# Kernel tuning notes

Hardware: AMD Instinct MI355X
Metric: run time of the kernel (lower is better)

## Reference

```python
import jax, jax.numpy as jnp
import numpy as np

B = 4; IMG = 32; P = 2; CIN = 3; G = IMG // P; N = G * G; D = 768; NL = 8
DI = 1536; NH = 24; HD = 64; DS = 128; CONVDIM = DI + 2 * DS; DPROJ = 2 * DI + 2 * DS + NH
OUTC = 3 * CIN; FREQ = 256; EPS = 1e-6


def _sincos_1d(dim, pos):
    omega = np.arange(dim // 2, dtype=np.float64) / (dim / 2.0)
    omega = 1.0 / 10000 ** omega
    out = np.einsum('m,d->md', pos.reshape(-1), omega)
    return np.concatenate([np.sin(out), np.cos(out)], axis=1)


def _pos_embed_2d(dim, gs):
    gh = np.arange(gs, dtype=np.float32)
    gw = np.arange(gs, dtype=np.float32)
    grid = np.stack(np.meshgrid(gw, gh), axis=0)
    return np.concatenate([_sincos_1d(dim // 2, grid[0]), _sincos_1d(dim // 2, grid[1])], axis=1)


POS = jnp.asarray(_pos_embed_2d(D, G), dtype=jnp.float32)[None]  # [1, N, D]


def _ln(x):
    m = x.mean(-1, keepdims=True)
    v = ((x - m) ** 2).mean(-1, keepdims=True)
    return (x - m) * jax.lax.rsqrt(v + EPS)


def _patch_embed(img, w, b):
    # conv with kernel=stride=P == reshape to (c, ph, pw)-ordered patch vectors + matmul
    xp = img.reshape(B, CIN, G, P, G, P).transpose(0, 2, 4, 1, 3, 5).reshape(B, N, CIN * P * P)
    return xp @ w + b


def _t_embed(t, tw1, tb1, tw2, tb2):
    half = FREQ // 2
    freqs = jnp.exp(-jnp.log(10000.0) * jnp.arange(half, dtype=jnp.float32) / half)
    args = t[:, None] * freqs[None]
    emb = jnp.concatenate([jnp.cos(args), jnp.sin(args)], axis=-1)
    return jax.nn.silu(emb @ tw1 + tb1) @ tw2 + tb2


def _mamba2(u, in_w, conv_w, conv_b, dt_bias, A_log, D_ssm, out_w):
    # u: [B, N, D]
    zxbcdt = u @ in_w                           # [B, N, DPROJ]
    z = zxbcdt[..., :DI]
    xBC = zxbcdt[..., DI:DI + CONVDIM]
    dt_raw = zxbcdt[..., DI + CONVDIM:]
    # causal depthwise conv1d, kernel 4
    pad = jnp.pad(xBC, ((0, 0), (3, 0), (0, 0)))
    xBC = sum(pad[:, k:k + N, :] * conv_w[:, k] for k in range(4)) + conv_b
    xBC = jax.nn.silu(xBC)
    xs = xBC[..., :DI].reshape(B, N, NH, HD)
    Bm = xBC[..., DI:DI + DS]
    Cm = xBC[..., DI + DS:]
    dt = jax.nn.softplus(dt_raw + dt_bias)       # [B, N, NH]
    a = dt * (-jnp.exp(A_log))                   # [B, N, NH], negative
    acum = jnp.cumsum(a, axis=1)
    seg = acum[:, :, None, :] - acum[:, None, :, :]   # [B, l, s, NH]
    tril = jnp.tril(jnp.ones((N, N), bool))
    decay = jnp.exp(jnp.where(tril[None, :, :, None], seg, -1e30))
    decay = jnp.moveaxis(decay, -1, 1)           # [B, NH, l, s]
    CB = jnp.einsum('bln,bsn->bls', Cm, Bm)
    scores = CB[:, None] * decay * jnp.moveaxis(dt, -1, 1)[:, :, None, :]
    y = jnp.einsum('bhls,bshp->blhp', scores, xs) + D_ssm[None, None, :, None] * xs
    y = y.reshape(B, N, DI) * jax.nn.silu(z)
    return y @ out_w


def _conv3(x, w, b):
    o = jax.lax.conv_general_dilated(x, w, (1, 1), 'SAME',
                                     dimension_numbers=('NCHW', 'OIHW', 'NCHW'))
    return o + b[None, :, None, None]


def _hfnet(h, w1, b1, w2, b2, w3, b3):
    c = jax.nn.relu(_conv3(h, w1, b1))
    c = jax.nn.relu(_conv3(c, w2, b2))
    return h + _conv3(c, w3, b3)


def _forward(x, t, y, H1, H2, H3, xe_w, xe_b, ye_w, ye_b, tw1, tb1, tw2, tb2,
             adaln_w, adaln_b, in_w, conv_w, conv_b, dt_bias, A_log, D_ssm, out_w,
             fl_t_w, fl_t_b, fl_y_w, fl_y_b, fl_lin_w, fl_lin_b,
             e1_w1, e1_b1, e1_w2, e1_b2, e1_w3, e1_b3,
             e2_w1, e2_b1, e2_w2, e2_b2, e2_w3, e2_b3,
             e3_w1, e3_b1, e3_w2, e3_b2, e3_w3, e3_b3):
    xe = _patch_embed(x, xe_w, xe_b) + POS
    ye = _patch_embed(y, ye_w, ye_b) + POS
    te = _t_embed(t, tw1, tb1, tw2, tb2)
    st = jax.nn.silu(te)          # [B, D]
    sy = jax.nn.silu(ye)          # [B, N, D]

    def layer(xc, p):
        aw, ab, iw, cw, cb, db, al, dd, ow = p
        sh_t, sc_t, g_t = jnp.split(st @ aw + ab, 3, axis=-1)
        sh_y, sc_y, g_y = jnp.split(sy @ aw + ab, 3, axis=-1)
        shift = sh_t[:, None] + sh_y
        scale = sc_t[:, None] + sc_y
        gate = g_t[:, None] + g_y
        xm = _ln(xc) * (1.0 + scale) + shift
        return gate * _mamba2(xm, iw, cw, cb, db, al, dd, ow) + xc, None

    xh, _ = jax.lax.scan(layer, xe, (adaln_w, adaln_b, in_w, conv_w, conv_b,
                                     dt_bias, A_log, D_ssm, out_w))
    sh_t, sc_t = jnp.split(st @ fl_t_w + fl_t_b, 2, axis=-1)
    sh_y, sc_y = jnp.split(sy @ fl_y_w + fl_y_b, 2, axis=-1)
    xf = (_ln(xh) * (1.0 + sc_t[:, None] + sc_y) + sh_t[:, None] + sh_y) @ fl_lin_w + fl_lin_b
    # unpatchify: nhwpqc -> nchpwq
    img = xf.reshape(B, G, G, P, P, OUTC).transpose(0, 5, 1, 3, 2, 4).reshape(B, OUTC, IMG, IMG)
    h1 = _hfnet(H1, e1_w1, e1_b1, e1_w2, e1_b2, e1_w3, e1_b3)
    h2 = _hfnet(H2, e2_w1, e2_b1, e2_w2, e2_b2, e2_w3, e2_b3)
    h3 = _hfnet(H3, e3_w1, e3_b1, e3_w2, e3_b2, e3_w3, e3_b3)
    return (img, h1, h2, h3)


def setup_inputs() -> dict:
    ks = iter(jax.random.split(jax.random.key(0), 80))
    def nrm(shape, s=0.02):
        return jax.random.normal(next(ks), shape, jnp.float32) * s
    z = lambda *s: jnp.zeros(s, jnp.float32)
    inp = {}
    inp['x'] = jax.random.normal(next(ks), (B, CIN, IMG, IMG), jnp.float32)
    inp['t'] = jax.random.uniform(next(ks), (B,), jnp.float32) * 1000.0
    inp['y'] = jax.random.normal(next(ks), (B, CIN, IMG, IMG), jnp.float32)
    inp['H1'] = jax.random.normal(next(ks), (B, CIN, IMG, IMG), jnp.float32)
    inp['H2'] = jax.random.normal(next(ks), (B, CIN, IMG, IMG), jnp.float32)
    inp['H3'] = jax.random.normal(next(ks), (B, CIN, IMG, IMG), jnp.float32)
    inp['xe_w'] = nrm((CIN * P * P, D), 0.1); inp['xe_b'] = z(D)
    inp['ye_w'] = nrm((CIN * P * P, D), 0.1); inp['ye_b'] = z(D)
    inp['tw1'] = nrm((FREQ, D)); inp['tb1'] = z(D)
    inp['tw2'] = nrm((D, D)); inp['tb2'] = z(D)
    inp['adaln_w'] = nrm((NL, D, 3 * D)); inp['adaln_b'] = nrm((NL, 3 * D))
    inp['in_w'] = nrm((NL, D, DPROJ))
    inp['conv_w'] = nrm((NL, CONVDIM, 4), 0.2); inp['conv_b'] = z(NL, CONVDIM)
    inp['dt_bias'] = nrm((NL, NH), 0.5)
    inp['A_log'] = jnp.tile(jnp.log(jnp.arange(1.0, NH + 1.0, dtype=jnp.float32)), (NL, 1))
    inp['D_ssm'] = jnp.ones((NL, NH), jnp.float32)
    inp['out_w'] = nrm((NL, DI, D))
    inp['fl_t_w'] = nrm((D, 2 * D)); inp['fl_t_b'] = z(2 * D)
    inp['fl_y_w'] = nrm((D, 2 * D)); inp['fl_y_b'] = z(2 * D)
    inp['fl_lin_w'] = nrm((D, P * P * OUTC)); inp['fl_lin_b'] = z(P * P * OUTC)
    for i in (1, 2, 3):
        inp['e%d_w1' % i] = nrm((64, CIN, 3, 3), 0.1); inp['e%d_b1' % i] = z(64)
        inp['e%d_w2' % i] = nrm((64, 64, 3, 3), 0.05); inp['e%d_b2' % i] = z(64)
        inp['e%d_w3' % i] = nrm((CIN, 64, 3, 3), 0.05); inp['e%d_b3' % i] = z(CIN)
    return inp


def reference(x, t, y, H1, H2, H3, xe_w, xe_b, ye_w, ye_b, tw1, tb1, tw2, tb2,
              adaln_w, adaln_b, in_w, conv_w, conv_b, dt_bias, A_log, D_ssm, out_w,
              fl_t_w, fl_t_b, fl_y_w, fl_y_b, fl_lin_w, fl_lin_b,
              e1_w1, e1_b1, e1_w2, e1_b2, e1_w3, e1_b3,
              e2_w1, e2_b1, e2_w2, e2_b2, e2_w3, e2_b3,
              e3_w1, e3_b1, e3_w2, e3_b2, e3_w3, e3_b3):
    return _forward(x, t, y, H1, H2, H3, xe_w, xe_b, ye_w, ye_b, tw1, tb1, tw2, tb2,
                    adaln_w, adaln_b, in_w, conv_w, conv_b, dt_bias, A_log, D_ssm, out_w,
                    fl_t_w, fl_t_b, fl_y_w, fl_y_b, fl_lin_w, fl_lin_b,
                    e1_w1, e1_b1, e1_w2, e1_b2, e1_w3, e1_b3,
                    e2_w1, e2_b1, e2_w2, e2_b2, e2_w3, e2_b3,
                    e3_w1, e3_b1, e3_w2, e3_b2, e3_w3, e3_b3)
```

## Files before the change

### kernel.cpp

```cpp
#include <hip/hip_runtime.h>
#include <cmath>

namespace {

constexpr int kB = 4;
constexpr int kN = 256;
constexpr int kD = 768;
constexpr int kNL = 8;
constexpr int kDI = 1536;
constexpr int kNH = 24;
constexpr int kHD = 64;
constexpr int kCONV = 1792;
constexpr int kDPROJ = 3352;
constexpr int kD3 = 2304;
constexpr int kNCAT = 19968;
constexpr int kOFF_FL = 18432;

typedef __attribute__((ext_vector_type(8))) short short8;
typedef __attribute__((ext_vector_type(4))) float f32x4;

__device__ __forceinline__ float siluf(float x) { return x / (1.f + expf(-x)); }

__device__ __forceinline__ short f2bf(float f) {
  unsigned u = __float_as_uint(f);
  unsigned r = (u + 0x7fffu + ((u >> 16) & 1u)) >> 16;
  return (short)r;
}

__device__ __forceinline__ void gload_lds16(const void* g, void* l) {
  __builtin_amdgcn_global_load_lds(
      (const __attribute__((address_space(1))) void*)g,
      (__attribute__((address_space(3))) void*)l, 16, 0, 0);
}

template <int N> __device__ __forceinline__ void wait_barrier();
template <> __device__ __forceinline__ void wait_barrier<0>() {
  asm volatile("s_waitcnt vmcnt(0)\n\ts_barrier" ::: "memory");
}
template <> __device__ __forceinline__ void wait_barrier<2>() {
  asm volatile("s_waitcnt vmcnt(2)\n\ts_barrier" ::: "memory");
}
template <> __device__ __forceinline__ void wait_barrier<3>() {
  asm volatile("s_waitcnt vmcnt(3)\n\ts_barrier" ::: "memory");
}
template <> __device__ __forceinline__ void wait_barrier<4>() {
  asm volatile("s_waitcnt vmcnt(4)\n\ts_barrier" ::: "memory");
}

__global__ void patch_embed2_kernel(const float* __restrict__ img0,
                                    const float* __restrict__ w0,
                                    const float* __restrict__ b0,
                                    float* __restrict__ out0,
                                    const float* __restrict__ img1,
                                    const float* __restrict__ w1,
                                    const float* __restrict__ b1,
                                    float* __restrict__ out1,
                                    short* __restrict__ out1_bf) {
  int gid = blockIdx.x * blockDim.x + threadIdx.x;
  if (gid >= kB * kN * kD) return;
  int z = blockIdx.z;
  const float* img = z ? img1 : img0;
  const float* w = z ? w1 : w0;
  const float* bias = z ? b1 : b0;
  int d = gid % kD;
  int n = (gid / kD) % kN;
  int b = gid / (kD * kN);
  int gi = n >> 4, gj = n & 15;
  float acc = bias[d];
#pragma unroll
  for (int c = 0; c < 3; ++c)
#pragma unroll
    for (int pi = 0; pi < 2; ++pi)
#pragma unroll
      for (int pj = 0; pj < 2; ++pj) {
        float v = img[((b * 3 + c) * 32 + gi * 2 + pi) * 32 + gj * 2 + pj];
        acc += v * w[(c * 4 + pi * 2 + pj) * kD + d];
      }
  float pos;
  if (d < 192)       pos = sinf((float)gj * powf(10000.f, -(float)d / 192.f));
  else if (d < 384)  pos = cosf((float)gj * powf(10000.f, -(float)(d - 192) / 192.f));
  else if (d < 576)  pos = sinf((float)gi * powf(10000.f, -(float)(d - 384) / 192.f));
  else               pos = cosf((float)gi * powf(10000.f, -(float)(d - 576) / 192.f));
  acc += pos;
  if (z) {
    float v = siluf(acc);
    out1[gid] = v;
    out1_bf[gid] = f2bf(v);
  } else {
    out0[gid] = acc;
  }
}

__global__ void tembed_args_kernel(const float* __restrict__ t,
                                   float* __restrict__ ctst) {
  int idx = blockIdx.x * 256 + threadIdx.x;
  if (idx >= kB * 256) return;
  int b = idx >> 8, j = idx & 255;
  int k = j & 127;
  float f = expf(-9.210340371976184f * (float)k / 128.f);
  float arg = t[b] * f;
  ctst[idx] = (j < 128) ? cosf(arg) : sinf(arg);
}

__global__ __launch_bounds__(256) void splitk_mm_stage1(
    const float* __restrict__ A, const float* __restrict__ W,
    float* __restrict__ part, int K, int Nn, int KC) {
  int n = blockIdx.x * 256 + threadIdx.x;
  int kc = blockIdx.y;
  int l = blockIdx.z;
  if (n >= Nn) return;
  const float* w = W + (size_t)l * K * Nn + (size_t)kc * 64 * Nn + n;
  int kb = kc * 64;
  float a0 = 0.f, a1 = 0.f, a2 = 0.f, a3 = 0.f;
  for (int k = 0; k < 64; ++k) {
    float wv = w[(size_t)k * Nn];
    a0 += A[0 * K + kb + k] * wv;
    a1 += A[1 * K + kb + k] * wv;
    a2 += A[2 * K + kb + k] * wv;
    a3 += A[3 * K + kb + k] * wv;
  }
  size_t base = (((size_t)l * KC + kc) * 4) * Nn + n;
  part[base] = a0;
  part[base + Nn] = a1;
  part[base + 2 * (size_t)Nn] = a2;
  part[base + 3 * (size_t)Nn] = a3;
}

__global__ void splitk_mm_reduce(const float* __restrict__ part,
                                 const float* __restrict__ bias,
                                 float* __restrict__ C, int Nn, int KC, int L,
                                 int act) {
  int idx = blockIdx.x * 256 + threadIdx.x;
  if (idx >= L * 4 * Nn) return;
  int n = idx % Nn;
  int b = (idx / Nn) & 3;
  int l = idx / (4 * Nn);
  float s = bias[(size_t)l * Nn + n];
  for (int kc = 0; kc < KC; ++kc)
    s += part[(((size_t)l * KC + kc) * 4 + b) * Nn + n];
  C[idx] = act ? siluf(s) : s;
}

__global__ __launch_bounds__(256) void transposeW_kernel(
    const float* __restrict__ W, short* __restrict__ Wt, int K, int N,
    size_t sW, size_t sWt) {
  W += (size_t)blockIdx.z * sW;
  Wt += (size_t)blockIdx.z * sWt;
  __shared__ float tile[32][33];
  int n0 = blockIdx.x * 32, k0 = blockIdx.y * 32;
  int tid = threadIdx.x;
  int tx = tid & 31, ty = tid >> 5;
#pragma unroll
  for (int i = 0; i < 4; ++i) {
    int k = k0 + ty + i * 8;
    int n = n0 + tx;
    tile[ty + i * 8][tx] = (n < N) ? W[(size_t)k * N + n] : 0.f;
  }
  __syncthreads();
#pragma unroll
  for (int i = 0; i < 4; ++i) {
    int n = n0 + ty + i * 8;
    int k = k0 + tx;
    Wt[(size_t)n * K + k] = f2bf(tile[tx][ty + i * 8]);
  }
}

__global__ void concat_bias_kernel(const float* __restrict__ a,
                                   const float* __restrict__ b,
                                   float* __restrict__ dst) {
  int i = blockIdx.x * 256 + threadIdx.x;
  if (i < kOFF_FL) dst[i] = a[i];
  else if (i < kNCAT) dst[i] = b[i - kOFF_FL];
}

template <int BM, int BN>
__global__ __launch_bounds__(256) void mfma_gemm(
    const short* __restrict__ A, const short* __restrict__ Bt,
    const float* __restrict__ bias, float* __restrict__ C,
    int Nn, int Ksplit, int Ktot, int ldc, size_t czstride) {
  constexpr int MI = BM / 32;
  constexpr int NJ = BN / 32;
  constexpr int LPW = BM / 64 + BN / 64;
  __shared__ short Als[3 * BM * 32];
  __shared__ short Bls[3 * BN * 32];
  int gx = gridDim.x, gy = gridDim.y;
  int nblk = gx * gy;
  int hl = blockIdx.y * gx + blockIdx.x;
  int txi, tyi;
  if ((nblk & 7) == 0) {
    int chunk = nblk >> 3;
    int s_id = (hl & 7) * chunk + (hl >> 3);
    txi = s_id / gy;
    tyi = s_id % gy;
  } else {
    txi = blockIdx.x;
    tyi = blockIdx.y;
  }
  int m0 = tyi * BM, n0 = txi * BN;
  int koff = blockIdx.z * Ksplit;
  C += (size_t)blockIdx.z * czstride;
  int tid = threadIdx.x;
  int lane = tid & 63, wid = tid >> 6;
  int wr = wid >> 1, wc = wid & 1;
  f32x4 acc[MI][NJ] = {};
  int sm = tid >> 2;
  int sk = (tid & 3) * 8;
  const int nsteps = Ksplit >> 5;
  auto stage = [&](int buf, int k0) {
#pragma unroll
    for (int h = 0; h < BM / 64; ++h)
      gload_lds16(&A[(size_t)(m0 + h * 64 + sm) * Ktot + koff + k0 + sk],
                  &Als[buf * (BM * 32) + h * 2048 + wid * 512]);
#pragma unroll
    for (int h = 0; h < BN / 64; ++h)
      gload_lds16(&Bt[(size_t)(n0 + h * 64 + sm) * Ktot + koff + k0 + sk],
                  &Bls[buf * (BN * 32) + h * 2048 + wid * 512]);
  };
  stage(0, 0);
  if (nsteps > 1) stage(1, 32);
  int cur = 0;
  for (int s = 0; s < nsteps; ++s) {
    if (s + 1 < nsteps) wait_barrier<LPW>();
    else wait_barrier<0>();
    if (s + 2 < nsteps) stage(cur == 0 ? 2 : cur - 1, (s + 2) << 5);
    short8 av[MI], bv[NJ];
#pragma unroll
    for (int mi = 0; mi < MI; ++mi)
      av[mi] = *(const short8*)&Als[cur * (BM * 32) +
                                    (wr * (BM / 2) + mi * 16 + (lane & 15)) *
                                        32 +
                                    (lane >> 4) * 8];
#pragma unroll
    for (int nj = 0; nj < NJ; ++nj)
      bv[nj] = *(const short8*)&Bls[cur * (BN * 32) +
                                    (wc * (BN / 2) + nj * 16 + (lane & 15)) *
                                        32 +
                                    (lane >> 4) * 8];
#pragma unroll
    for (int mi = 0; mi < MI; ++mi)
#pragma unroll
      for (int nj = 0; nj < NJ; ++nj)
        acc[mi][nj] = __builtin_amdgcn_mfma_f32_16x16x32_bf16(
            av[mi], bv[nj], acc[mi][nj], 0, 0, 0);
    cur = (cur == 2) ? 0 : cur + 1;
  }
#pragma unroll
  for (int mi = 0; mi < MI; ++mi)
#pragma unroll
    for (int nj = 0; nj < NJ; ++nj)
#pragma unroll
      for (int r = 0; r < 4; ++r) {
        int gm = m0 + wr * (BM / 2) + mi * 16 + (lane >> 4) * 4 + r;
        int gn = n0 + wc * (BN / 2) + nj * 16 + (lane & 15);
        if (gn >= Nn) continue;
        C[(size_t)gm * ldc + gn] = acc[mi][nj][r] + (bias ? bias[gn] : 0.f);
      }
}

__global__ __launch_bounds__(256) void cb_mfma_kernel(
    const short* __restrict__ bC, const short* __restrict__ bB,
    float* __restrict__ CBp) {
  constexpr int K = 128;
  __shared__ short Als[128 * 32];
  __shared__ short Bls[128 * 32];
  int b = blockIdx.z;
  int m0 = blockIdx.y * 128, n0 = blockIdx.x * 128;
  if (n0 >= m0 + 128) return;
  const short* A = bC + (size_t)b * 256 * K;
  const short* Bt = bB + (size_t)b * 256 * K;
  int tid = threadIdx.x;
  int lane = tid & 63, wid = tid >> 6;
  int wr = wid >> 1, wc = wid & 1;
  f32x4 acc[4][4] = {};
  int sm = tid >> 2;
  int sk = (tid & 3) * 8;
  for (int k0 = 0; k0 < K; k0 += 32) {
    __syncthreads();
    gload_lds16(&A[(size_t)(m0 + sm) * K + k0 + sk], &Als[wid * 512]);
    gload_lds16(&A[(size_t)(m0 + 64 + sm) * K + k0 + sk],
                &Als[2048 + wid * 512]);
    gload_lds16(&Bt[(size_t)(n0 + sm) * K + k0 + sk], &Bls[wid * 512]);
    gload_lds16(&Bt[(size_t)(n0 + 64 + sm) * K + k0 + sk],
                &Bls[2048 + wid * 512]);
    __syncthreads();
    short8 av[4], bv[4];
#pragma unroll
    for (int mi = 0; mi < 4; ++mi)
      av[mi] = *(const short8*)&Als[(wr * 64 + mi * 16 + (lane & 15)) * 32 +
                                    (lane >> 4) * 8];
#pragma unroll
    for (int nj = 0; nj < 4; ++nj)
      bv[nj] = *(const short8*)&Bls[(wc * 64 + nj * 16 + (lane & 15)) * 32 +
                                    (lane >> 4) * 8];
#pragma unroll
    for (int mi = 0; mi < 4; ++mi)
#pragma unroll
      for (int nj = 0; nj < 4; ++nj)
        acc[mi][nj] = __builtin_amdgcn_mfma_f32_16x16x32_bf16(
            av[mi], bv[nj], acc[mi][nj], 0, 0, 0);
  }
#pragma unroll
  for (int mi = 0; mi < 4; ++mi)
#pragma unroll
    for (int nj = 0; nj < 4; ++nj)
#pragma unroll
      for (int r = 0; r < 4; ++r) {
        int gm = m0 + wr * 64 + mi * 16 + (lane >> 4) * 4 + r;
        int gn = n0 + wc * 64 + nj * 16 + (lane & 15);
        CBp[((size_t)(b * 256 + gm)) * 256 + gn] = acc[mi][nj][r];
      }
}

__global__ __launch_bounds__(256) void ln_mod_kernel(
    const float* __restrict__ x, const float* __restrict__ tA,
    const float* __restrict__ yA, short* __restrict__ out_bf, int tstride,
    int ystride, const float* __restrict__ p0, const float* __restrict__ p1,
    const float* __restrict__ gtA, const float* __restrict__ gyA,
    float* __restrict__ xcw) {
  int row = blockIdx.x;
  int b = row >> 8;
  __shared__ float xr[kD];
  __shared__ float red[256];
  int tid = threadIdx.x;
  float s = 0.f;
  for (int i = tid; i < kD; i += 256) {
    float v = x[(size_t)row * kD + i];
    if (p0) {
      float g = gtA[b * kD3 + 2 * kD + i] +
                gyA[(size_t)row * kNCAT + 2 * kD + i];
      v += g * (p0[(size_t)row * kD + i] + p1[(size_t)row * kD + i]);
      xcw[(size_t)row * kD + i] = v;
    }
    xr[i] = v;
    s += v;
  }
  red[tid] = s;
  __syncthreads();
  for (int o = 128; o > 0; o >>= 1) {
    if (tid < o) red[tid] += red[tid + o];
    __syncthreads();
  }
  float mean = red[0] / (float)kD;
  __syncthreads();
  float s2 = 0.f;
  for (int i = tid; i < kD; i += 256) {
    float d = xr[i] - mean;
    s2 += d * d;
  }
  red[tid] = s2;
  __syncthreads();
  for (int o = 128; o > 0; o >>= 1) {
    if (tid < o) red[tid] += red[tid + o];
    __syncthreads();
  }
  float rstd = rsqrtf(red[0] / (float)kD + 1e-6f);
  for (int i = tid; i < kD; i += 256) {
    float sc = tA[b * tstride + kD + i] + yA[(size_t)row * ystride + kD + i];
    float sh = tA[b * tstride + i] + yA[(size_t)row * ystride + i];
    float v = (xr[i] - mean) * rstd * (1.f + sc) + sh;
    out_bf[(size_t)row * kD + i] = f2bf(v);
  }
}

__global__ __launch_bounds__(256) void convdt_kernel(
    const float* __restrict__ zx, const float* __restrict__ cw,
    const float* __restrict__ cb, const float* __restrict__ db,
    const float* __restrict__ al, float* __restrict__ xbc,
    short* __restrict__ bB, short* __restrict__ bC, float* __restrict__ dts,
    float* __restrict__ acum) {
  constexpr int kConvBlocks = kB * kN * kCONV / 256;
  int blk = blockIdx.x;
  if (blk < kConvBlocks) {
    int idx = blk * 256 + threadIdx.x;
    int c = idx % kCONV;
    int row = idx / kCONV;
    int n = row & 255, b = row >> 8;
    float acc = cb[c];
#pragma unroll
    for (int k = 0; k < 4; ++k) {
      int ns = n + k - 3;
      if (ns >= 0)
        acc += zx[(size_t)(b * kN + ns) * kDPROJ + kDI + c] * cw[c * 4 + k];
    }
    float v = siluf(acc);
    xbc[idx] = v;
    if (c >= kDI) {
      if (c < kDI + 128)
        bB[(size_t)row * 128 + (c - kDI)] = f2bf(v);
      else
        bC[(size_t)row * 128 + (c - kDI - 128)] = f2bf(v);
    }
  } else {
    int bh = blk - kConvBlocks;
    int b = bh / kNH, h = bh % kNH;
    int n = threadIdx.x;
    __shared__ float sb[256];
    size_t row = (size_t)(b * kN + n);
    float xv = zx[row * kDPROJ + (kDI + kCONV) + h] + db[h];
    float dt = xv > 20.f ? xv : log1pf(expf(xv));
    dts[row * kNH + h] = dt;
    float a = -expf(al[h]) * dt;
    sb[n] = a;
    __syncthreads();
    for (int off = 1; off < 256; off <<= 1) {
      float v = (n >= off) ? sb[n - off] : 0.f;
      __syncthreads();
      sb[n] += v;
      __syncthreads();
    }
    acum[row * kNH + h] = sb[n];
  }
}

__global__ __launch_bounds__(256) void ssm_y_kernel(
    const float* __restrict__ CBp, const float* __restrict__ acum,
    const float* __restrict__ dts, const float* __restrict__ xbc,
    const float* __restrict__ zx, const float* __restrict__ Dssm,
    short* __restrict__ ybuf) {
  int bh = blockIdx.z;
  int b = bh / kNH, h = bh % kNH;
  int m0 = blockIdx.y * 64;
  int tid = threadIdx.x;
  int tx = tid & 15, ty = tid >> 4;
  __shared__ float As[16][65];
  __shared__ float Xs[16][64];
  float acc[4][4] = {};
  for (int k0 = 0; k0 < kN; k0 += 16) {
    if (k0 > m0 + 63) break;
#pragma unroll
    for (int i = 0; i < 4; ++i) {
      int e = tid + i * 256;
      int m = e >> 4, k = e & 15;
      int l = m0 + m, ss = k0 + k;
      float v = 0.f;
      if (ss <= l) {
        float dec = expf(acum[(size_t)(b * kN + l) * kNH + h] -
                         acum[(size_t)(b * kN + ss) * kNH + h]);
        v = CBp[(size_t)(b * kN + l) * kN + ss] * dec *
            dts[(size_t)(b * kN + ss) * kNH + h];
      }
      As[k][m] = v;
    }
#pragma unroll
    for (int i = 0; i < 4; ++i) {
      int e = tid + i * 256;
      int k = e >> 6, n = e & 63;
      Xs[k][n] = xbc[(size_t)(b * kN + k0 + k) * kCONV + h * kHD + n];
    }
    __syncthreads();
#pragma unroll
    for (int kk = 0; kk < 16; ++kk) {
      float a[4], bb[4];
#pragma unroll
      for (int i = 0; i < 4; ++i) a[i] = As[kk][ty * 4 + i];
#pragma unroll
      for (int j = 0; j < 4; ++j) bb[j] = Xs[kk][tx * 4 + j];
#pragma unroll
      for (int i = 0; i < 4; ++i)
#pragma unroll
        for (int j = 0; j < 4; ++j) acc[i][j] += a[i] * bb[j];
    }
    __syncthreads();
  }
  float dd = Dssm[h];
#pragma unroll
  for (int i = 0; i < 4; ++i) {
    int l = m0 + ty * 4 + i;
    size_t row = (size_t)(b * kN + l);
#pragma unroll
    for (int j = 0; j < 4; ++j) {
      int p = tx * 4 + j;
      int col = h * kHD + p;
      float xs_l = xbc[row * kCONV + col];
      float yv = acc[i][j] + dd * xs_l;
      float zv = zx[row * kDPROJ + col];
      ybuf[row * kDI + col] = f2bf(yv * siluf(zv));
    }
  }
}

__global__ void unpatchify_kernel(const float* __restrict__ fpp,
                                  const float* __restrict__ bias,
                                  float* __restrict__ out) {
  constexpr int kFP = kB * kN * 36;
  int gid = blockIdx.x * 256 + threadIdx.x;
  if (gid >= kFP) return;
  int j = gid % 36;
  int row = gid / 36;
  int n = row & 255, b = row >> 8;
  int o = j % 9;
  int pj = (j / 9) & 1;
  int pi = j / 18;
  int gi = n >> 4, gj = n & 15;
  float v = fpp[gid] + fpp[kFP + gid] + fpp[2 * kFP + gid] +
            fpp[3 * kFP + gid] + bias[j];
  out[((b * 9 + o) * 32 + gi * 2 + pi) * 32 + (gj * 2 + pj)] = v;
}

__global__ __launch_bounds__(256) void conv1_kernel(
    const float* __restrict__ Ha, const float* __restrict__ Hb,
    const float* __restrict__ Hc, const float* __restrict__ wa,
    const float* __restrict__ wb, const float* __restrict__ wc,
    const float* __restrict__ ba, const float* __restrict__ bb,
    const float* __restrict__ bc, short* __restrict__ dst) {
  int gid = blockIdx.x * 256 + threadIdx.x;
  if (gid >= 3 * 4096 * 64) return;
  int oc = gid & 63;
  int px = (gid >> 6) & 4095;
  int net = gid >> 18;
  const float* in = net == 0 ? Ha : (net == 1 ? Hb : Hc);
  const float* w = net == 0 ? wa : (net == 1 ? wb : wc);
  const float* bs = net == 0 ? ba : (net == 1 ? bb : bc);
  int xx = px & 31, yy = (px >> 5) & 31, b = px >> 10;
  float acc = bs[oc];
#pragma unroll
  for (int ic = 0; ic < 3; ++ic) {
    const float* ip = in + ((size_t)(b * 3 + ic) << 10);
    const float* wp = w + (oc * 3 + ic) * 9;
#pragma unroll
    for (int ky = 0; ky < 3; ++ky) {
      int ys = yy + ky - 1;
      if (ys < 0 || ys > 31) continue;
#pragma unroll
      for (int kx = 0; kx < 3; ++kx) {
        int xs = xx + kx - 1;
        if (xs < 0 || xs > 31) continue;
        acc += ip[ys * 32 + xs] * wp[ky * 3 + kx];
      }
    }
  }
  dst[gid] = f2bf(fmaxf(acc, 0.f));
}

__global__ __launch_bounds__(256) void convw_prep_kernel(
    const float* __restrict__ w2a, const float* __restrict__ w2b,
    const float* __restrict__ w2c, const float* __restrict__ w3a,
    const float* __restrict__ w3b, const float* __restrict__ w3c,
    short* __restrict__ dst2, short* __restrict__ dst3) {
  int idx = blockIdx.x * 256 + threadIdx.x;
  if (idx >= 3 * 128 * 576) return;
  int z = blockIdx.z;
  int OC = z ? 3 : 64;
  short* dst = z ? dst3 : dst2;
  int k = idx % 576;
  int row = (idx / 576) & 127;
  int net = idx / (128 * 576);
  const float* w = z ? (net == 0 ? w3a : (net == 1 ? w3b : w3c))
                     : (net == 0 ? w2a : (net == 1 ? w2b : w2c));
  int pos = k >> 6, ic = k & 63;
  float v = (row < OC) ? w[row * 576 + ic * 9 + pos] : 0.f;
  dst[idx] = f2bf(v);
}

template <int EP>
__global__ __launch_bounds__(256) void conv_gemm(
    const short* __restrict__ src, const short* __restrict__ Btall,
    const float* __restrict__ b_a, const float* __restrict__ b_b,
    const float* __restrict__ b_c, const float* __restrict__ r_a,
    const float* __restrict__ r_b, const float* __restrict__ r_c,
    short* __restrict__ dst, float* __restrict__ outp) {
  constexpr int K = 576;
  __shared__ short Als[128 * 32];
  __shared__ short Bls[128 * 32];
  int net = blockIdx.z;
  int m0 = blockIdx.y * 128;
  const float* bias = net == 0 ? b_a : (net == 1 ? b_b : b_c);
  const float* res = net == 0 ? r_a : (net == 1 ? r_b : r_c);
  const short* Bt = Btall + (size_t)net * 128 * K;
  int tid = threadIdx.x;
  int lane = tid & 63, wid = tid >> 6;
  int wr = wid >> 1, wc = wid & 1;
  f32x4 acc[4][4] = {};
  int sm = tid >> 2;
  int sk = (tid & 3) * 8;
  for (int k0 = 0; k0 < K; k0 += 32) {
    int kk = k0 + sk;
    int pos = kk >> 6, ic0 = kk & 63;
    int ky = pos / 3 - 1, kx = pos % 3 - 1;
    uint4 a_st[2], b_st[2];
#pragma unroll
    for (int i = 0; i < 2; ++i) {
      int px = m0 + i * 64 + sm;
      int b = px >> 10;
      int yy = (px >> 5) & 31, xx = px & 31;
      int ys = yy + ky, xs = xx + kx;
      if (ys >= 0 && ys < 32 && xs >= 0 && xs < 32) {
        a_st[i] = *(const uint4*)&src[((size_t)(net * 4096 + (b << 10) +
                                                (ys << 5) + xs)
                                       << 6) +
                                      ic0];
      } else {
        a_st[i] = make_uint4(0u, 0u, 0u, 0u);
      }
      b_st[i] = *(const uint4*)&Bt[(size_t)(i * 64 + sm) * K + kk];
    }
    __syncthreads();
    *(uint4*)&Als[sm * 32 + sk] = a_st[0];
    *(uint4*)&Als[(64 + sm) * 32 + sk] = a_st[1];
    *(uint4*)&Bls[sm * 32 + sk] = b_st[0];
    *(uint4*)&Bls[(64 + sm) * 32 + sk] = b_st[1];
    __syncthreads();
    short8 av[4], bv[4];
#pragma unroll
    for (int mi = 0; mi < 4; ++mi)
      av[mi] = *(const short8*)&Als[(wr * 64 + mi * 16 + (lane & 15)) * 32 +
                                    (lane >> 4) * 8];
#pragma unroll
    for (int nj = 0; nj < 4; ++nj)
      bv[nj] = *(const short8*)&Bls[(wc * 64 + nj * 16 + (lane & 15)) * 32 +
                                    (lane >> 4) * 8];
#pragma unroll
    for (int mi = 0; mi < 4; ++mi)
#pragma unroll
      for (int nj = 0; nj < 4; ++nj)
        acc[mi][nj] = __builtin_amdgcn_mfma_f32_16x16x32_bf16(
            av[mi], bv[nj], acc[mi][nj], 0, 0, 0);
  }
#pragma unroll
  for (int mi = 0; mi < 4; ++mi)
#pragma unroll
    for (int nj = 0; nj < 4; ++nj)
#pragma unroll
      for (int r = 0; r < 4; ++r) {
        int gm = m0 + wr * 64 + mi * 16 + (lane >> 4) * 4 + r;
        int gn = wc * 64 + nj * 16 + (lane & 15);
        float v = acc[mi][nj][r];
        if (EP == 0) {
          if (gn < 64)
            dst[(size_t)(net * 4096 + gm) * 64 + gn] =
                f2bf(fmaxf(v + bias[gn], 0.f));
        } else {
          if (gn < 3) {
            int b = gm >> 10, pix = gm & 1023;
            size_t o = (size_t)(b * 3 + gn) * 1024 + pix;
            outp[36864 + net * 12288 + o] = v + bias[gn] + res[o];
          }
        }
      }
}

}

extern "C" void kernel_launch(void* const* d_in, const int* in_sizes, int n_in,
                              void* d_out, int out_size, void* d_ws,
                              size_t ws_size, hipStream_t stream) {
  const float* x = (const float*)d_in[0];
  const float* t = (const float*)d_in[1];
  const float* y = (const float*)d_in[2];
  const float* H[3] = {(const float*)d_in[3], (const float*)d_in[4],
                       (const float*)d_in[5]};
  const float* xe_w = (const float*)d_in[6];
  const float* xe_b = (const float*)d_in[7];
  const float* ye_w = (const float*)d_in[8];
  const float* ye_b = (const float*)d_in[9];
  const float* tw1 = (const float*)d_in[10];
  const float* tb1 = (const float*)d_in[11];
  const float* tw2 = (const float*)d_in[12];
  const float* tb2 = (const float*)d_in[13];
  const float* adaln_w = (const float*)d_in[14];
  const float* adaln_b = (const float*)d_in[15];
  const float* in_w = (const float*)d_in[16];
  const float* conv_w = (const float*)d_in[17];
  const float* conv_b = (const float*)d_in[18];
  const float* dt_bias = (const float*)d_in[19];
  const float* A_log = (const float*)d_in[20];
  const float* D_ssm = (const float*)d_in[21];
  const float* out_w = (const float*)d_in[22];
  const float* fl_t_w = (const float*)d_in[23];
  const float* fl_t_b = (const float*)d_in[24];
  const float* fl_y_w = (const float*)d_in[25];
  const float* fl_y_b = (const float*)d_in[26];
  const float* fl_lin_w = (const float*)d_in[27];
  const float* fl_lin_b = (const float*)d_in[28];

  float* out = (float*)d_out;
  float* ws = (float*)d_ws;

  size_t off = 0;
  auto alloc = [&](size_t nelem) { float* p = ws + off; off += nelem; return p; };
  float* xc    = alloc((size_t)kB * kN * kD);
  float* sy    = alloc((size_t)kB * kN * kD);
  short* sy_bf = (short*)alloc((size_t)kB * kN * kD / 2);
  float* st    = alloc((size_t)kB * kD);
  float* ht    = alloc((size_t)kB * kD);
  float* ctst  = alloc((size_t)kB * 256);
  float* tAall = alloc((size_t)kNL * kB * kD3);
  float* yA8   = alloc((size_t)kB * kN * kNCAT);
  short* xm_bf = (short*)alloc((size_t)kB * kN * kD / 2);
  float* zx    = alloc((size_t)kB * kN * kDPROJ);
  float* xbc   = alloc((size_t)kB * kN * kCONV);
  float* dts   = alloc((size_t)kB * kN * kNH);
  float* acum  = alloc((size_t)kB * kN * kNH);
  float* CBp   = alloc((size_t)kB * kN * kN);
  short* ybuf  = (short*)alloc((size_t)kB * kN * kDI / 2);
  float* tfl   = alloc((size_t)kB * 2 * kD);
  float* opart = alloc((size_t)2 * kB * kN * kD);
  float* fpp   = alloc((size_t)4 * kB * kN * 36);
  short* adalnT = (short*)alloc((size_t)kNCAT * kD / 2);
  float* biascat = alloc(kNCAT);
  short* in_wT = (short*)alloc((size_t)kNL * 3456 * kD / 2);
  short* Wt    = (short*)alloc((size_t)128 * kD / 2);
  short* bBm   = (short*)alloc((size_t)kB * kN * 128 / 2);
  short* bCm   = (short*)alloc((size_t)kB * kN * 128 / 2);
  short* c1bf  = (short*)alloc((size_t)3 * 4096 * 64 / 2);
  short* c2bf  = (short*)alloc((size_t)3 * 4096 * 64 / 2);
  short* Bt2   = (short*)alloc((size_t)3 * 128 * 576 / 2);
  short* Bt3   = (short*)alloc((size_t)3 * 128 * 576 / 2);
  (void)ws_size;

  float* part = zx;
  short* out_wT = adalnT;

  dim3 blk(256);

  patch_embed2_kernel<<<dim3((kB * kN * kD + 255) / 256, 1, 2), blk, 0,
                        stream>>>(x, xe_w, xe_b, xc, y, ye_w, ye_b, sy, sy_bf);

  transposeW_kernel<<<dim3(72, 24, kNL), blk, 0, stream>>>(
      adaln_w, adalnT, kD, kD3, (size_t)kD * kD3, (size_t)kD3 * kD);
  transposeW_kernel<<<dim3(48, 24, 1), blk, 0, stream>>>(
      fl_y_w, adalnT + (size_t)kOFF_FL * kD, kD, 2 * kD, 0, 0);
  concat_bias_kernel<<<dim3((kNCAT + 255) / 256), blk, 0, stream>>>(
      adaln_b, fl_y_b, biascat);
  mfma_gemm<128, 128><<<dim3(kNCAT / 128, 8), blk, 0, stream>>>(
      sy_bf, adalnT, biascat, yA8, kNCAT, kD, kD, kNCAT, 0);

  transposeW_kernel<<<dim3(108, 24, kNL), blk, 0, stream>>>(
      in_w, in_wT, kD, kDPROJ, (size_t)kD * kDPROJ, (size_t)3456 * kD);
  transposeW_kernel<<<dim3(24, 48, kNL), blk, 0, stream>>>(
      out_w, out_wT, kDI, kD, (size_t)kDI * kD, (size_t)768 * kDI);

  tembed_args_kernel<<<dim3(4), blk, 0, stream>>>(t, ctst);
  splitk_mm_stage1<<<dim3(3, 4, 1), blk, 0, stream>>>(ctst, tw1, part, 256,
                                                      kD, 4);
  splitk_mm_reduce<<<dim3((kB * kD + 255) / 256), blk, 0, stream>>>(
      part, tb1, ht, kD, 4, 1, 1);
  splitk_mm_stage1<<<dim3(3, 12, 1), blk, 0, stream>>>(ht, tw2, part, kD, kD, 12);
  splitk_mm_reduce<<<dim3((kB * kD + 255) / 256), blk, 0, stream>>>(
      part, tb2, st, kD, 12, 1, 1);
  splitk_mm_stage1<<<dim3(9, 12, kNL), blk, 0, stream>>>(st, adaln_w, part, kD,
                                                         kD3, 12);
  splitk_mm_reduce<<<dim3((kNL * kB * kD3 + 255) / 256), blk, 0, stream>>>(
      part, adaln_b, tAall, kD3, 12, kNL, 0);
  splitk_mm_stage1<<<dim3(6, 12, 1), blk, 0, stream>>>(st, fl_t_w, part, kD,
                                                       2 * kD, 12);
  splitk_mm_reduce<<<dim3((kB * 2 * kD + 255) / 256), blk, 0, stream>>>(
      part, fl_t_b, tfl, 2 * kD, 12, 1, 0);

  for (int l = 0; l < kNL; ++l) {
    const float* cw = conv_w + (size_t)l * kCONV * 4;
    const float* cb = conv_b + (size_t)l * kCONV;
    const float* db = dt_bias + (size_t)l * kNH;
    const float* al = A_log + (size_t)l * kNH;
    const float* dd = D_ssm + (size_t)l * kNH;
    float* tA = tAall + (size_t)l * kB * kD3;
    const float* yAl = yA8 + (size_t)l * kD3;
    const float* ptA = l ? tAall + (size_t)(l - 1) * kB * kD3 : nullptr;
    const float* pyA = l ? yA8 + (size_t)(l - 1) * kD3 : nullptr;

    ln_mod_kernel<<<dim3(kB * kN), blk, 0, stream>>>(
        xc, tA, yAl, xm_bf, kD3, kNCAT, l ? opart : nullptr,
        l ? opart + (size_t)kB * kN * kD : nullptr, ptA, pyA, xc);
    mfma_gemm<64, 64><<<dim3(54, 16), blk, 0, stream>>>(
        xm_bf, in_wT + (size_t)l * 3456 * kD, nullptr, zx, kDPROJ, kD, kD,
        kDPROJ, 0);
    convdt_kernel<<<dim3(kB * kN * kCONV / 256 + kB * kNH), blk, 0, stream>>>(
        zx, cw, cb, db, al, xbc, bBm, bCm, dts, acum);
    cb_mfma_kernel<<<dim3(2, 2, kB), blk, 0, stream>>>(bCm, bBm, CBp);
    ssm_y_kernel<<<dim3(1, kN / 64, kB * kNH), blk, 0, stream>>>(
        CBp, acum, dts, xbc, zx, dd, ybuf);
    mfma_gemm<64, 64><<<dim3(12, 16, 2), blk, 0, stream>>>(
        ybuf, out_wT + (size_t)l * 768 * kDI, nullptr, opart, kD, kD, kDI,
        kD, (size_t)kB * kN * kD);
  }

  ln_mod_kernel<<<dim3(kB * kN), blk, 0, stream>>>(
      xc, tfl, yA8 + kOFF_FL, xm_bf, 2 * kD, kNCAT, opart,
      opart + (size_t)kB * kN * kD, tAall + (size_t)7 * kB * kD3,
      yA8 + (size_t)7 * kD3, xc);
  transposeW_kernel<<<dim3(4, 24, 1), blk, 0, stream>>>(fl_lin_w, Wt, kD, 36,
                                                        0, 0);
  mfma_gemm<64, 128><<<dim3(1, 16, 4), blk, 0, stream>>>(
      xm_bf, Wt, nullptr, fpp, 36, 192, kD, 36, (size_t)kB * kN * 36);
  unpatchify_kernel<<<dim3((kB * kN * 36 + 255) / 256), blk, 0, stream>>>(
      fpp, fl_lin_b, out);

  const float* w1s[3] = {(const float*)d_in[29], (const float*)d_in[35],
                         (const float*)d_in[41]};
  const float* b1s[3] = {(const float*)d_in[30], (const float*)d_in[36],
                         (const float*)d_in[42]};
  const float* w2s[3] = {(const float*)d_in[31], (const float*)d_in[37],
                         (const float*)d_in[43]};
  const float* b2s[3] = {(const float*)d_in[32], (const float*)d_in[38],
                         (const float*)d_in[44]};
  const float* w3s[3] = {(const float*)d_in[33], (const float*)d_in[39],
                         (const float*)d_in[45]};
  const float* b3s[3] = {(const float*)d_in[34], (const float*)d_in[40],
                         (const float*)d_in[46]};
  convw_prep_kernel<<<dim3((3 * 128 * 576 + 255) / 256, 1, 2), blk, 0,
                      stream>>>(w2s[0], w2s[1], w2s[2], w3s[0], w3s[1],
                                w3s[2], Bt2, Bt3);
  conv1_kernel<<<dim3(3 * 4096 * 64 / 256), blk, 0, stream>>>(
      H[0], H[1], H[2], w1s[0], w1s[1], w1s[2], b1s[0], b1s[1], b1s[2], c1bf);
  conv_gemm<0><<<dim3(1, 32, 3), blk, 0, stream>>>(
      c1bf, Bt2, b2s[0], b2s[1], b2s[2], nullptr, nullptr, nullptr, c2bf,
      nullptr);
  conv_gemm<1><<<dim3(1, 32, 3), blk, 0, stream>>>(
      c2bf, Bt3, b3s[0], b3s[1], b3s[2], H[0], H[1], H[2], nullptr, out);
}
```

Baseline: 1.141 ms.

## Fuse C·B score MFMA into SSM kernel and use wave-shuffle LayerNorm reductions

Removes the separate cb_mfma kernel and its fp32 CBp buffer. Each SSM block now computes its 16x16 C·B tiles on the fly with MFMA directly from the bf16 B/C arrays, and applies the decay and dt weighting in registers before writing to LDS. This drops one launch per layer and a global write/read round trip, but every head block redoes the C·B product, which is shared across heads. Separately, the LayerNorm kernel keeps the row in registers and reduces with wave shuffles instead of an LDS tree with many barriers.

```diff
diff --git a/kernel.cpp b/kernel.cpp
--- a/kernel.cpp
+++ b/kernel.cpp
@@ -257,60 +257,6 @@
       }
 }
 
-__global__ __launch_bounds__(256) void cb_mfma_kernel(
-    const short* __restrict__ bC, const short* __restrict__ bB,
-    float* __restrict__ CBp) {
-  constexpr int K = 128;
-  __shared__ short Als[128 * 32];
-  __shared__ short Bls[128 * 32];
-  int b = blockIdx.z;
-  int m0 = blockIdx.y * 128, n0 = blockIdx.x * 128;
-  if (n0 >= m0 + 128) return;
-  const short* A = bC + (size_t)b * 256 * K;
-  const short* Bt = bB + (size_t)b * 256 * K;
-  int tid = threadIdx.x;
-  int lane = tid & 63, wid = tid >> 6;
-  int wr = wid >> 1, wc = wid & 1;
-  f32x4 acc[4][4] = {};
-  int sm = tid >> 2;
-  int sk = (tid & 3) * 8;
-  for (int k0 = 0; k0 < K; k0 += 32) {
-    __syncthreads();
-    gload_lds16(&A[(size_t)(m0 + sm) * K + k0 + sk], &Als[wid * 512]);
-    gload_lds16(&A[(size_t)(m0 + 64 + sm) * K + k0 + sk],
-                &Als[2048 + wid * 512]);
-    gload_lds16(&Bt[(size_t)(n0 + sm) * K + k0 + sk], &Bls[wid * 512]);
-    gload_lds16(&Bt[(size_t)(n0 + 64 + sm) * K + k0 + sk],
-                &Bls[2048 + wid * 512]);
-    __syncthreads();
-    short8 av[4], bv[4];
-#pragma unroll
-    for (int mi = 0; mi < 4; ++mi)
-      av[mi] = *(const short8*)&Als[(wr * 64 + mi * 16 + (lane & 15)) * 32 +
-                                    (lane >> 4) * 8];
-#pragma unroll
-    for (int nj = 0; nj < 4; ++nj)
-      bv[nj] = *(const short8*)&Bls[(wc * 64 + nj * 16 + (lane & 15)) * 32 +
-                                    (lane >> 4) * 8];
-#pragma unroll
-    for (int mi = 0; mi < 4; ++mi)
-#pragma unroll
-      for (int nj = 0; nj < 4; ++nj)
-        acc[mi][nj] = __builtin_amdgcn_mfma_f32_16x16x32_bf16(
-            av[mi], bv[nj], acc[mi][nj], 0, 0, 0);
-  }
-#pragma unroll
-  for (int mi = 0; mi < 4; ++mi)
-#pragma unroll
-    for (int nj = 0; nj < 4; ++nj)
-#pragma unroll
-      for (int r = 0; r < 4; ++r) {
-        int gm = m0 + wr * 64 + mi * 16 + (lane >> 4) * 4 + r;
-        int gn = n0 + wc * 64 + nj * 16 + (lane & 15);
-        CBp[((size_t)(b * 256 + gm)) * 256 + gn] = acc[mi][nj][r];
-      }
-}
-
 __global__ __launch_bounds__(256) void ln_mod_kernel(
     const float* __restrict__ x, const float* __restrict__ tA,
     const float* __restrict__ yA, short* __restrict__ out_bf, int tstride,
@@ -319,11 +265,13 @@
     float* __restrict__ xcw) {
   int row = blockIdx.x;
   int b = row >> 8;
-  __shared__ float xr[kD];
-  __shared__ float red[256];
   int tid = threadIdx.x;
+  __shared__ float w1[4], w2[4];
+  float xr[3];
   float s = 0.f;
-  for (int i = tid; i < kD; i += 256) {
+#pragma unroll
+  for (int k = 0; k < 3; ++k) {
+    int i = tid + k * 256;
     float v = x[(size_t)row * kD + i];
     if (p0) {
       float g = gtA[b * kD3 + 2 * kD + i] +
@@ -331,33 +279,31 @@
       v += g * (p0[(size_t)row * kD + i] + p1[(size_t)row * kD + i]);
       xcw[(size_t)row * kD + i] = v;
     }
-    xr[i] = v;
+    xr[k] = v;
     s += v;
   }
-  red[tid] = s;
+#pragma unroll
+  for (int o = 32; o > 0; o >>= 1) s += __shfl_down(s, o, 64);
+  if ((tid & 63) == 0) w1[tid >> 6] = s;
   __syncthreads();
-  for (int o = 128; o > 0; o >>= 1) {
-    if (tid < o) red[tid] += red[tid + o];
-    __syncthreads();
-  }
-  float mean = red[0] / (float)kD;
+  float mean = (w1[0] + w1[1] + w1[2] + w1[3]) * (1.f / kD);
+  float s2 = 0.f;
+#pragma unroll
+  for (int k = 0; k < 3; ++k) {
+    float d = xr[k] - mean;
+    s2 += d * d;
+  }
+#pragma unroll
+  for (int o = 32; o > 0; o >>= 1) s2 += __shfl_down(s2, o, 64);
+  if ((tid & 63) == 0) w2[tid >> 6] = s2;
   __syncthreads();
-  float s2 = 0.f;
-  for (int i = tid; i < kD; i += 256) {
-    float d = xr[i] - mean;
-    s2 += d * d;
-  }
-  red[tid] = s2;
-  __syncthreads();
-  for (int o = 128; o > 0; o >>= 1) {
-    if (tid < o) red[tid] += red[tid + o];
-    __syncthreads();
-  }
-  float rstd = rsqrtf(red[0] / (float)kD + 1e-6f);
-  for (int i = tid; i < kD; i += 256) {
+  float rstd = rsqrtf((w2[0] + w2[1] + w2[2] + w2[3]) * (1.f / kD) + 1e-6f);
+#pragma unroll
+  for (int k = 0; k < 3; ++k) {
+    int i = tid + k * 256;
     float sc = tA[b * tstride + kD + i] + yA[(size_t)row * ystride + kD + i];
     float sh = tA[b * tstride + i] + yA[(size_t)row * ystride + i];
-    float v = (xr[i] - mean) * rstd * (1.f + sc) + sh;
+    float v = (xr[k] - mean) * rstd * (1.f + sc) + sh;
     out_bf[(size_t)row * kD + i] = f2bf(v);
   }
 }
@@ -413,39 +359,54 @@
 }
 
 __global__ __launch_bounds__(256) void ssm_y_kernel(
-    const float* __restrict__ CBp, const float* __restrict__ acum,
-    const float* __restrict__ dts, const float* __restrict__ xbc,
-    const float* __restrict__ zx, const float* __restrict__ Dssm,
-    short* __restrict__ ybuf) {
+    const short* __restrict__ bCm, const short* __restrict__ bBm,
+    const float* __restrict__ acum, const float* __restrict__ dts,
+    const float* __restrict__ xbc, const float* __restrict__ zx,
+    const float* __restrict__ Dssm, short* __restrict__ ybuf) {
   int bh = blockIdx.z;
   int b = bh / kNH, h = bh % kNH;
   int m0 = blockIdx.y * 64;
   int tid = threadIdx.x;
+  int lane = tid & 63, wid = tid >> 6;
   int tx = tid & 15, ty = tid >> 4;
   __shared__ float As[16][65];
   __shared__ float Xs[16][64];
   float acc[4][4] = {};
+  float acum_l[4];
+#pragma unroll
+  for (int r = 0; r < 4; ++r) {
+    int l = m0 + wid * 16 + (lane >> 4) * 4 + r;
+    acum_l[r] = acum[(size_t)(b * kN + l) * kNH + h];
+  }
+  const short* cRow =
+      &bCm[((size_t)(b * kN + m0 + wid * 16 + (lane & 15))) * 128 +
+           (lane >> 4) * 8];
   for (int k0 = 0; k0 < kN; k0 += 16) {
     if (k0 > m0 + 63) break;
-#pragma unroll
-    for (int i = 0; i < 4; ++i) {
-      int e = tid + i * 256;
-      int m = e >> 4, k = e & 15;
-      int l = m0 + m, ss = k0 + k;
-      float v = 0.f;
-      if (ss <= l) {
-        float dec = expf(acum[(size_t)(b * kN + l) * kNH + h] -
-                         acum[(size_t)(b * kN + ss) * kNH + h]);
-        v = CBp[(size_t)(b * kN + l) * kN + ss] * dec *
-            dts[(size_t)(b * kN + ss) * kNH + h];
-      }
-      As[k][m] = v;
-    }
+    f32x4 cb = {};
+    const short* bRow =
+        &bBm[((size_t)(b * kN + k0 + (lane & 15))) * 128 + (lane >> 4) * 8];
+#pragma unroll
+    for (int ks = 0; ks < 4; ++ks)
+      cb = __builtin_amdgcn_mfma_f32_16x16x32_bf16(
+          *(const short8*)(cRow + ks * 32), *(const short8*)(bRow + ks * 32),
+          cb, 0, 0, 0);
+    int ss = k0 + (lane & 15);
+    float acum_ss = acum[(size_t)(b * kN + ss) * kNH + h];
+    float dts_ss = dts[(size_t)(b * kN + ss) * kNH + h];
 #pragma unroll
     for (int i = 0; i < 4; ++i) {
       int e = tid + i * 256;
       int k = e >> 6, n = e & 63;
       Xs[k][n] = xbc[(size_t)(b * kN + k0 + k) * kCONV + h * kHD + n];
+    }
+#pragma unroll
+    for (int r = 0; r < 4; ++r) {
+      int mloc = wid * 16 + (lane >> 4) * 4 + r;
+      int l = m0 + mloc;
+      float v = 0.f;
+      if (ss <= l) v = cb[r] * expf(acum_l[r] - acum_ss) * dts_ss;
+      As[lane & 15][mloc] = v;
     }
     __syncthreads();
 #pragma unroll
@@ -691,7 +652,6 @@
   float* xbc   = alloc((size_t)kB * kN * kCONV);
   float* dts   = alloc((size_t)kB * kN * kNH);
   float* acum  = alloc((size_t)kB * kN * kNH);
-  float* CBp   = alloc((size_t)kB * kN * kN);
   short* ybuf  = (short*)alloc((size_t)kB * kN * kDI / 2);
   float* tfl   = alloc((size_t)kB * 2 * kD);
   float* opart = alloc((size_t)2 * kB * kN * kD);
@@ -766,9 +726,8 @@
         kDPROJ, 0);
     convdt_kernel<<<dim3(kB * kN * kCONV / 256 + kB * kNH), blk, 0, stream>>>(
         zx, cw, cb, db, al, xbc, bBm, bCm, dts, acum);
-    cb_mfma_kernel<<<dim3(2, 2, kB), blk, 0, stream>>>(bCm, bBm, CBp);
     ssm_y_kernel<<<dim3(1, kN / 64, kB * kNH), blk, 0, stream>>>(
-        CBp, acum, dts, xbc, zx, dd, ybuf);
+        bCm, bBm, acum, dts, xbc, zx, dd, ybuf);
     mfma_gemm<64, 64><<<dim3(12, 16, 2), blk, 0, stream>>>(
         ybuf, out_wT + (size_t)l * 768 * kDI, nullptr, opart, kD, kD, kDI,
         kD, (size_t)kB * kN * kD);
```

After: 1.031 ms. 9.7% less time.
